# Kernel optimization log

Hardware: AMD Instinct MI355X
Metric: run time of the kernel (lower is better)

## Reference

```python
import jax, jax.numpy as jnp
import numpy as np

ALPHA_1 = 1.0
ALPHA_2 = 1.0

def setup_inputs() -> dict:
    key = jax.random.key(0)
    k1, k2, k3, k4 = jax.random.split(key, 4)
    n, d = 4096, 1024
    # xavier_normal-ish scale for (d,d): std = sqrt(2/(d+d)) = 1/sqrt(d)
    s = 1.0 / np.sqrt(d)
    Y = jax.random.normal(k1, (n, d), dtype=jnp.float32)
    W = jax.random.normal(k2, (d, d), dtype=jnp.float32) * s
    Wf = jax.random.normal(k3, (d, d), dtype=jnp.float32) * s
    B = jax.random.normal(k4, (1, d), dtype=jnp.float32) * s
    return {"Y": Y, "W": W, "Wf": Wf, "B": B}

def reference(Y, W, Wf, B):
    # Attention: scores = Y @ (W^T W) @ Y^T = (Y W^T)(Y W^T)^T
    YWt = Y @ W.T                      # (n, d)
    A = jax.nn.softmax(YWt @ YWt.T, axis=-1)  # (n, n)
    Z = (1.0 - ALPHA_1) * Y + ALPHA_1 * (A @ Y)  # (n, d); alpha_1=1 -> A@Y
    # FFN: Wf_eff = -0.5*alpha_2*(Wf + Wf^T) + (1-alpha_2)*I; alpha_2=1
    d = Wf.shape[0]
    Wf_eff = -0.5 * ALPHA_2 * (Wf + Wf.T) + (1.0 - ALPHA_2) * jnp.eye(d, dtype=Wf.dtype)
    out = Z @ Wf_eff + B               # (n, d)
    out = jax.nn.relu(out)             # relu=True
    return out
```

## Files before the change

### kernel.cpp

```cpp
#include <hip/hip_runtime.h>
#include <cstdint>
#include <cmath>


typedef __attribute__((ext_vector_type(8))) short short8;
typedef __attribute__((ext_vector_type(4))) short short4v;
typedef __attribute__((ext_vector_type(4))) float f32x4;

__device__ __forceinline__ short f2bf(float x) {
    unsigned u = __builtin_bit_cast(unsigned, x);
    u += 0x7fffu + ((u >> 16) & 1u);
    return (short)(u >> 16);
}
__device__ __forceinline__ float bf2f(short s) {
    unsigned u = ((unsigned)(unsigned short)s) << 16;
    return __builtin_bit_cast(float, u);
}

typedef const __attribute__((address_space(1))) void* gas1_t;
typedef __attribute__((address_space(3))) void* las3_t;
__device__ __forceinline__ void cp16(const void* g, void* l) {
    __builtin_amdgcn_global_load_lds((gas1_t)(uintptr_t)g, (las3_t)(uintptr_t)l, 16, 0, 0);
}

template<bool SPLIT, int OUTMODE, bool SYMM>
__global__ __launch_bounds__(256)
void mfma_gemm(const short* __restrict__ Ah, const short* __restrict__ Al,
               const short* __restrict__ Bh, const short* __restrict__ Bl,
               const float* __restrict__ bias, void* Co_, void* Cl_,
               int M, int N, int K)
{
    constexpr int BK = SPLIT ? 32 : 64;
    constexpr int NT = SPLIT ? 4 : 2;
    constexpr int TS = 128 * BK;
    __shared__ short lds[2][NT][TS];

    const int tid  = threadIdx.x;
    const int lane = tid & 63;
    const int wave = tid >> 6;
    const int wr   = wave >> 1, wc = wave & 1;

    int bm, bn, bi = 0, bj = 0;
    if (SYMM) {
        const int NB = N >> 7;
        int lin = blockIdx.x;
        const int nwg = gridDim.x;
        if ((nwg & 7) == 0) lin = (lin & 7) * (nwg >> 3) + (lin >> 3);
        const float ff = (float)(2 * NB + 1);
        int i = (int)((ff - sqrtf(ff * ff - 8.0f * (float)lin)) * 0.5f);
        while ((i + 1) * (2 * NB - i) / 2 <= lin) ++i;
        while (i * (2 * NB - i + 1) / 2 > lin) --i;
        bi = i;
        bj = i + (lin - i * (2 * NB - i + 1) / 2);
        bm = bi << 7; bn = bj << 7;
    } else {
        const int gx  = gridDim.x;
        const int nwg = gx * gridDim.y;
        int lin = blockIdx.y * gx + blockIdx.x;
        if ((nwg & 7) == 0) { const int cpx = nwg >> 3; lin = (lin & 7) * cpx + (lin >> 3); }
        bm = (lin / gx) << 7;
        bn = (lin % gx) << 7;
    }

    f32x4 acc[4][4];
#pragma unroll
    for (int i = 0; i < 4; ++i)
#pragma unroll
        for (int j = 0; j < 4; ++j)
#pragma unroll
            for (int q = 0; q < 4; ++q) acc[i][j][q] = 0.f;

    const short *pA0, *pA1, *pA2, *pA3, *pB0, *pB1, *pB2, *pB3;
    if constexpr (SPLIT) {
        const int srow = tid >> 2;
        const int csw  = (tid & 3) ^ ((tid >> 3) & 3);
        const size_t oA = (size_t)(bm + srow) * K + csw * 8;
        const size_t oB = (size_t)(bn + srow) * K + csw * 8;
        pA0 = Ah + oA; pA1 = Ah + oA + (size_t)64 * K;
        pA2 = Al + oA; pA3 = Al + oA + (size_t)64 * K;
        pB0 = Bh + oB; pB1 = Bh + oB + (size_t)64 * K;
        pB2 = Bl + oB; pB3 = Bl + oB + (size_t)64 * K;
    } else {
        const int srow = tid >> 3;
        const int lch  = (tid & 7) ^ (srow & 7);
        const size_t oA = (size_t)(bm + srow) * K + lch * 8;
        const size_t oB = (size_t)(bn + srow) * K + lch * 8;
        pA0 = Ah + oA; pA1 = pA0 + (size_t)32 * K;
        pA2 = pA0 + (size_t)64 * K; pA3 = pA0 + (size_t)96 * K;
        pB0 = Bh + oB; pB1 = pB0 + (size_t)32 * K;
        pB2 = pB0 + (size_t)64 * K; pB3 = pB0 + (size_t)96 * K;
    }

    auto stage = [&](int buf, int t) {
        short* db = &lds[buf][0][0] + tid * 8;
        const int ko = t * BK;
        if constexpr (SPLIT) {
            cp16(pA0 + ko, db);                cp16(pA1 + ko, db + 2048);
            cp16(pA2 + ko, db + 4096);         cp16(pA3 + ko, db + 4096 + 2048);
            cp16(pB0 + ko, db + 8192);         cp16(pB1 + ko, db + 8192 + 2048);
            cp16(pB2 + ko, db + 12288);        cp16(pB3 + ko, db + 12288 + 2048);
        } else {
            cp16(pA0 + ko, db);         cp16(pA1 + ko, db + 2048);
            cp16(pA2 + ko, db + 4096);  cp16(pA3 + ko, db + 6144);
            cp16(pB0 + ko, db + 8192);  cp16(pB1 + ko, db + 8192 + 2048);
            cp16(pB2 + ko, db + 8192 + 4096);  cp16(pB3 + ko, db + 8192 + 6144);
        }
    };

    int aoff, boff;
    if constexpr (SPLIT) {
        const int fsw = ((lane >> 4) ^ ((lane >> 1) & 3)) * 8;
        aoff = (wr * 64 + (lane & 15)) * 32 + fsw;
        boff = (wc * 64 + (lane & 15)) * 32 + fsw;
    } else {
        aoff = (wr * 64 + (lane & 15)) * 64;
        boff = (wc * 64 + (lane & 15)) * 64;
    }

    const int nt = K / BK;
    int cur = 0;

    stage(0, 0);
    asm volatile("s_waitcnt vmcnt(0)" ::: "memory");
    __syncthreads();

    for (int t = 0; t < nt; ++t) {
        if (t + 1 < nt) stage(cur ^ 1, t + 1);
        const short* base = &lds[cur][0][0];
        if constexpr (SPLIT) {
            short8 fah[4], fal[4], fbh[4], fbl[4];
#pragma unroll
            for (int i = 0; i < 4; ++i) {
                fah[i] = *(const short8*)(base + aoff + i * 512);
                fal[i] = *(const short8*)(base + 4096 + aoff + i * 512);
            }
#pragma unroll
            for (int j = 0; j < 4; ++j) {
                fbh[j] = *(const short8*)(base + 8192 + boff + j * 512);
                fbl[j] = *(const short8*)(base + 12288 + boff + j * 512);
            }
#pragma unroll
            for (int i = 0; i < 4; ++i)
#pragma unroll
                for (int j = 0; j < 4; ++j) {
                    acc[i][j] = __builtin_amdgcn_mfma_f32_16x16x32_bf16(fah[i], fbh[j], acc[i][j], 0, 0, 0);
                    acc[i][j] = __builtin_amdgcn_mfma_f32_16x16x32_bf16(fah[i], fbl[j], acc[i][j], 0, 0, 0);
                    acc[i][j] = __builtin_amdgcn_mfma_f32_16x16x32_bf16(fal[i], fbh[j], acc[i][j], 0, 0, 0);
                }
        } else {
#pragma unroll
            for (int ks = 0; ks < 2; ++ks) {
                const int sw = ((ks * 4 + (lane >> 4)) ^ (lane & 7)) * 8;
                short8 fa[4], fb[4];
#pragma unroll
                for (int i = 0; i < 4; ++i)
                    fa[i] = *(const short8*)(base + aoff + sw + i * 1024);
#pragma unroll
                for (int j = 0; j < 4; ++j)
                    fb[j] = *(const short8*)(base + 8192 + boff + sw + j * 1024);
#pragma unroll
                for (int i = 0; i < 4; ++i)
#pragma unroll
                    for (int j = 0; j < 4; ++j)
                        acc[i][j] = __builtin_amdgcn_mfma_f32_16x16x32_bf16(fa[i], fb[j], acc[i][j], 0, 0, 0);
            }
        }
        asm volatile("s_waitcnt vmcnt(0)" ::: "memory");
        __syncthreads();
        cur ^= 1;
    }

    const int crow0 = bm + wr * 64 + ((lane >> 4) << 2);
    const int ccol0 = bn + wc * 64 + (lane & 15);
    if constexpr (OUTMODE == 2) {
        float* C = (float*)Co_;
#pragma unroll
        for (int j = 0; j < 4; ++j) {
            const int c = ccol0 + j * 16;
            const float bv = bias[c];
#pragma unroll
            for (int i = 0; i < 4; ++i)
#pragma unroll
                for (int q = 0; q < 4; ++q) {
                    const int r = crow0 + i * 16 + q;
                    C[(size_t)r * N + c] = fmaxf(acc[i][j][q] + bv, 0.f);
                }
        }
    } else if constexpr (OUTMODE == 1) {
        short* Ch = (short*)Co_;
#pragma unroll
        for (int j = 0; j < 4; ++j) {
            const int c = ccol0 + j * 16;
#pragma unroll
            for (int i = 0; i < 4; ++i)
#pragma unroll
                for (int q = 0; q < 4; ++q) {
                    const int r = crow0 + i * 16 + q;
                    Ch[(size_t)r * N + c] = f2bf(acc[i][j][q]);
                }
        }
    } else {
        short* Ch = (short*)Co_;
        short* Cl = (short*)Cl_;
        const bool mirror = SYMM && (bi != bj);
#pragma unroll
        for (int j = 0; j < 4; ++j) {
            const int c = ccol0 + j * 16;
#pragma unroll
            for (int i = 0; i < 4; ++i)
#pragma unroll
                for (int q = 0; q < 4; ++q) {
                    const int r = crow0 + i * 16 + q;
                    const float v = acc[i][j][q];
                    const short hh = f2bf(v);
                    const short ll = f2bf(v - bf2f(hh));
                    Ch[(size_t)r * N + c] = hh;
                    Cl[(size_t)r * N + c] = ll;
                    if (mirror) {
                        Ch[(size_t)c * N + r] = hh;
                        Cl[(size_t)c * N + r] = ll;
                    }
                }
        }
    }
}

__global__ __launch_bounds__(256)
void softmax_hi(short* __restrict__ Shi, const short* __restrict__ Slo)
{
    const int row = blockIdx.x;
    short8* ph = (short8*)(Shi + (size_t)row * 4096);
    const short8* pl = (const short8*)(Slo + (size_t)row * 4096);
    const int t = threadIdx.x;

    short8 h0 = ph[t], h1 = ph[t + 256];
    short8 l0 = pl[t], l1 = pl[t + 256];
    float x[16];
#pragma unroll
    for (int j = 0; j < 8; ++j) {
        x[j]     = bf2f(h0[j]) + bf2f(l0[j]);
        x[8 + j] = bf2f(h1[j]) + bf2f(l1[j]);
    }
    float mx = x[0];
#pragma unroll
    for (int j = 1; j < 16; ++j) mx = fmaxf(mx, x[j]);
#pragma unroll
    for (int off = 32; off > 0; off >>= 1) mx = fmaxf(mx, __shfl_xor(mx, off));

    __shared__ float rm[4], rs[4];
    const int wv = t >> 6, ln = t & 63;
    if (ln == 0) rm[wv] = mx;
    __syncthreads();
    mx = fmaxf(fmaxf(rm[0], rm[1]), fmaxf(rm[2], rm[3]));

    float s = 0.f;
#pragma unroll
    for (int j = 0; j < 16; ++j) { x[j] = __expf(x[j] - mx); s += x[j]; }
#pragma unroll
    for (int off = 32; off > 0; off >>= 1) s += __shfl_xor(s, off);
    if (ln == 0) rs[wv] = s;
    __syncthreads();
    s = rs[0] + rs[1] + rs[2] + rs[3];

    const float inv = 1.f / s;
    short8 o0, o1;
#pragma unroll
    for (int j = 0; j < 8; ++j) {
        o0[j] = f2bf(x[j] * inv);
        o1[j] = f2bf(x[8 + j] * inv);
    }
    ph[t] = o0; ph[t + 256] = o1;
}

__global__ __launch_bounds__(256)
void split_y(const float* __restrict__ Y, short* __restrict__ Yhi,
             short* __restrict__ Ylo, short* __restrict__ Yt)
{
    __shared__ float tb[64][65];
    const int rb = blockIdx.y * 64, cb = blockIdx.x * 64;
    const int t = threadIdx.x;
    const int r = t >> 4, c4 = (t & 15) * 4;
#pragma unroll
    for (int it = 0; it < 4; ++it) {
        const int row = rb + r + it * 16;
        const float4 v = *(const float4*)&Y[(size_t)row * 1024 + cb + c4];
        const float f[4] = {v.x, v.y, v.z, v.w};
        short4v h, l;
#pragma unroll
        for (int k = 0; k < 4; ++k) {
            const short hh = f2bf(f[k]);
            h[k] = hh;
            l[k] = f2bf(f[k] - bf2f(hh));
        }
        *(short4v*)&Yhi[(size_t)row * 1024 + cb + c4] = h;
        *(short4v*)&Ylo[(size_t)row * 1024 + cb + c4] = l;
        tb[r + it * 16][c4 + 0] = v.x; tb[r + it * 16][c4 + 1] = v.y;
        tb[r + it * 16][c4 + 2] = v.z; tb[r + it * 16][c4 + 3] = v.w;
    }
    __syncthreads();
    const int orow = t >> 2, oc0 = (t & 3) * 16;
    short8 h8[2];
#pragma unroll
    for (int g = 0; g < 2; ++g)
#pragma unroll
        for (int j = 0; j < 8; ++j)
            h8[g][j] = f2bf(tb[oc0 + g * 8 + j][orow]);
    const size_t ob = (size_t)(cb + orow) * 4096 + rb + oc0;
    *(short8*)&Yt[ob] = h8[0];
    *(short8*)&Yt[ob + 8] = h8[1];
}

__global__ __launch_bounds__(256)
void split_w(const float* __restrict__ Wm, short* __restrict__ Wh, short* __restrict__ Wl)
{
    const size_t idx = ((size_t)blockIdx.x * 256 + threadIdx.x) * 4;
    const float4 v = *(const float4*)&Wm[idx];
    const float f[4] = {v.x, v.y, v.z, v.w};
    short4v h, l;
#pragma unroll
    for (int k = 0; k < 4; ++k) {
        const short hh = f2bf(f[k]);
        h[k] = hh;
        l[k] = f2bf(f[k] - bf2f(hh));
    }
    *(short4v*)&Wh[idx] = h;
    *(short4v*)&Wl[idx] = l;
}

__global__ __launch_bounds__(256)
void symm_hi(const float* __restrict__ Wf, short* __restrict__ Fh)
{
    const int i  = blockIdx.x;
    const int j0 = threadIdx.x * 4;
    const float4 rv = *(const float4*)&Wf[(size_t)i * 1024 + j0];
    const float c0 = Wf[(size_t)(j0 + 0) * 1024 + i];
    const float c1 = Wf[(size_t)(j0 + 1) * 1024 + i];
    const float c2 = Wf[(size_t)(j0 + 2) * 1024 + i];
    const float c3 = Wf[(size_t)(j0 + 3) * 1024 + i];
    short4v h;
    h[0] = f2bf(-0.5f * (rv.x + c0));
    h[1] = f2bf(-0.5f * (rv.y + c1));
    h[2] = f2bf(-0.5f * (rv.z + c2));
    h[3] = f2bf(-0.5f * (rv.w + c3));
    *(short4v*)&Fh[(size_t)i * 1024 + j0] = h;
}

extern "C" void kernel_launch(void* const* d_in, const int* in_sizes, int n_in,
                              void* d_out, int out_size, void* d_ws, size_t ws_size,
                              hipStream_t stream)
{
    const float* Y  = (const float*)d_in[0];
    const float* W  = (const float*)d_in[1];
    const float* Wf = (const float*)d_in[2];
    const float* Bb = (const float*)d_in[3];
    float* out = (float*)d_out;

    const int n = 4096, d = 1024;

    char* w = (char*)d_ws;
    short* Ythi = (short*)w; w += (size_t)d * n * 2;
    short* Wfeh = (short*)w; w += (size_t)d * d * 2;
    short* YWth = (short*)w; w += (size_t)n * d * 2;
    short* YWtl = (short*)w; w += (size_t)n * d * 2;
    short* Shi  = (short*)w; w += (size_t)n * n * 2;
    short* Slo  = (short*)w; w += (size_t)n * n * 2;
    short* Yhi = Shi;
    short* Ylo = Yhi + (size_t)n * d;
    short* Whi = Ylo + (size_t)n * d;
    short* Wlo = Whi + (size_t)d * d;
    short* Zhi = YWth;

    split_y<<<dim3(16, 64), 256, 0, stream>>>(Y, Yhi, Ylo, Ythi);
    split_w<<<dim3(1024), 256, 0, stream>>>(W, Whi, Wlo);
    symm_hi<<<dim3(1024), 256, 0, stream>>>(Wf, Wfeh);

    mfma_gemm<true, 0, false><<<dim3(8, 32), 256, 0, stream>>>(
        Yhi, Ylo, Whi, Wlo, nullptr, YWth, YWtl, n, d, d);

    mfma_gemm<true, 0, true><<<dim3(528), 256, 0, stream>>>(
        YWth, YWtl, YWth, YWtl, nullptr, Shi, Slo, n, n, d);

    softmax_hi<<<dim3(n), 256, 0, stream>>>(Shi, Slo);

    mfma_gemm<false, 1, false><<<dim3(8, 32), 256, 0, stream>>>(
        Shi, nullptr, Ythi, nullptr, nullptr, Zhi, nullptr, n, d, n);

    mfma_gemm<false, 2, false><<<dim3(8, 32), 256, 0, stream>>>(
        Zhi, nullptr, Wfeh, nullptr, Bb, out, nullptr, n, d, d);
}
```

Before: 306.4 us.

## Use 8-wave 512-thread GEMM blocks with 64x32 per-wave tiles

```diff
diff --git a/kernel.cpp b/kernel.cpp
--- a/kernel.cpp
+++ b/kernel.cpp
@@ -24,21 +24,20 @@
 }
 
 template<bool SPLIT, int OUTMODE, bool SYMM>
-__global__ __launch_bounds__(256)
+__global__ __launch_bounds__(512, 4)
 void mfma_gemm(const short* __restrict__ Ah, const short* __restrict__ Al,
                const short* __restrict__ Bh, const short* __restrict__ Bl,
                const float* __restrict__ bias, void* Co_, void* Cl_,
                int M, int N, int K)
 {
     constexpr int BK = SPLIT ? 32 : 64;
-    constexpr int NT = SPLIT ? 4 : 2;
-    constexpr int TS = 128 * BK;
-    __shared__ short lds[2][NT][TS];
+    __shared__ short lds[2][16384];
 
     const int tid  = threadIdx.x;
     const int lane = tid & 63;
     const int wave = tid >> 6;
-    const int wr   = wave >> 1, wc = wave & 1;
+    const int wr   = wave >> 2;
+    const int wc   = wave & 3;
 
     int bm, bn, bi = 0, bj = 0;
     if (SYMM) {
@@ -62,59 +61,48 @@
         bn = (lin % gx) << 7;
     }
 
-    f32x4 acc[4][4];
-#pragma unroll
-    for (int i = 0; i < 4; ++i)
-#pragma unroll
-        for (int j = 0; j < 4; ++j)
-#pragma unroll
-            for (int q = 0; q < 4; ++q) acc[i][j][q] = 0.f;
-
-    const short *pA0, *pA1, *pA2, *pA3, *pB0, *pB1, *pB2, *pB3;
+    f32x4 acc[4][2];
+#pragma unroll
+    for (int m = 0; m < 4; ++m)
+#pragma unroll
+        for (int n = 0; n < 2; ++n)
+#pragma unroll
+            for (int q = 0; q < 4; ++q) acc[m][n][q] = 0.f;
+
+    const short *pA0, *pA1, *pB0, *pB1;
     if constexpr (SPLIT) {
-        const int srow = tid >> 2;
-        const int csw  = (tid & 3) ^ ((tid >> 3) & 3);
-        const size_t oA = (size_t)(bm + srow) * K + csw * 8;
-        const size_t oB = (size_t)(bn + srow) * K + csw * 8;
-        pA0 = Ah + oA; pA1 = Ah + oA + (size_t)64 * K;
-        pA2 = Al + oA; pA3 = Al + oA + (size_t)64 * K;
-        pB0 = Bh + oB; pB1 = Bh + oB + (size_t)64 * K;
-        pB2 = Bl + oB; pB3 = Bl + oB + (size_t)64 * K;
+        const int row = tid >> 2;
+        const int csw = (tid & 3) ^ ((tid >> 3) & 3);
+        const size_t oA = (size_t)(bm + row) * K + csw * 8;
+        const size_t oB = (size_t)(bn + row) * K + csw * 8;
+        pA0 = Ah + oA; pA1 = Al + oA;
+        pB0 = Bh + oB; pB1 = Bl + oB;
     } else {
-        const int srow = tid >> 3;
-        const int lch  = (tid & 7) ^ (srow & 7);
-        const size_t oA = (size_t)(bm + srow) * K + lch * 8;
-        const size_t oB = (size_t)(bn + srow) * K + lch * 8;
-        pA0 = Ah + oA; pA1 = pA0 + (size_t)32 * K;
-        pA2 = pA0 + (size_t)64 * K; pA3 = pA0 + (size_t)96 * K;
-        pB0 = Bh + oB; pB1 = pB0 + (size_t)32 * K;
-        pB2 = pB0 + (size_t)64 * K; pB3 = pB0 + (size_t)96 * K;
+        const int row = tid >> 3;
+        const int lch = (tid & 7) ^ ((tid >> 3) & 7);
+        const size_t oA = (size_t)(bm + row) * K + lch * 8;
+        const size_t oB = (size_t)(bn + row) * K + lch * 8;
+        pA0 = Ah + oA; pA1 = pA0 + (size_t)64 * K;
+        pB0 = Bh + oB; pB1 = pB0 + (size_t)64 * K;
     }
 
     auto stage = [&](int buf, int t) {
-        short* db = &lds[buf][0][0] + tid * 8;
+        short* db = &lds[buf][0] + tid * 8;
         const int ko = t * BK;
-        if constexpr (SPLIT) {
-            cp16(pA0 + ko, db);                cp16(pA1 + ko, db + 2048);
-            cp16(pA2 + ko, db + 4096);         cp16(pA3 + ko, db + 4096 + 2048);
-            cp16(pB0 + ko, db + 8192);         cp16(pB1 + ko, db + 8192 + 2048);
-            cp16(pB2 + ko, db + 12288);        cp16(pB3 + ko, db + 12288 + 2048);
-        } else {
-            cp16(pA0 + ko, db);         cp16(pA1 + ko, db + 2048);
-            cp16(pA2 + ko, db + 4096);  cp16(pA3 + ko, db + 6144);
-            cp16(pB0 + ko, db + 8192);  cp16(pB1 + ko, db + 8192 + 2048);
-            cp16(pB2 + ko, db + 8192 + 4096);  cp16(pB3 + ko, db + 8192 + 6144);
-        }
+        cp16(pA0 + ko, db);
+        cp16(pA1 + ko, db + 4096);
+        cp16(pB0 + ko, db + 8192);
+        cp16(pB1 + ko, db + 12288);
     };
 
     int aoff, boff;
     if constexpr (SPLIT) {
-        const int fsw = ((lane >> 4) ^ ((lane >> 1) & 3)) * 8;
-        aoff = (wr * 64 + (lane & 15)) * 32 + fsw;
-        boff = (wc * 64 + (lane & 15)) * 32 + fsw;
+        const int swz = ((lane >> 4) ^ ((lane >> 1) & 3)) * 8;
+        aoff = (wr * 64 + (lane & 15)) * 32 + swz;
+        boff = (wc * 32 + (lane & 15)) * 32 + swz;
     } else {
         aoff = (wr * 64 + (lane & 15)) * 64;
-        boff = (wc * 64 + (lane & 15)) * 64;
+        boff = (wc * 32 + (lane & 15)) * 64;
     }
 
     const int nt = K / BK;
@@ -126,43 +114,41 @@
 
     for (int t = 0; t < nt; ++t) {
         if (t + 1 < nt) stage(cur ^ 1, t + 1);
-        const short* base = &lds[cur][0][0];
+        const short* base = &lds[cur][0];
         if constexpr (SPLIT) {
-            short8 fah[4], fal[4], fbh[4], fbl[4];
-#pragma unroll
-            for (int i = 0; i < 4; ++i) {
-                fah[i] = *(const short8*)(base + aoff + i * 512);
-                fal[i] = *(const short8*)(base + 4096 + aoff + i * 512);
+            short8 fah[4], fal[4];
+#pragma unroll
+            for (int m = 0; m < 4; ++m) {
+                fah[m] = *(const short8*)(base + aoff + m * 512);
+                fal[m] = *(const short8*)(base + 4096 + aoff + m * 512);
             }
 #pragma unroll
-            for (int j = 0; j < 4; ++j) {
-                fbh[j] = *(const short8*)(base + 8192 + boff + j * 512);
-                fbl[j] = *(const short8*)(base + 12288 + boff + j * 512);
+            for (int n = 0; n < 2; ++n) {
+                const short8 fbh = *(const short8*)(base + 8192 + boff + n * 512);
+                const short8 fbl = *(const short8*)(base + 12288 + boff + n * 512);
+#pragma unroll
+                for (int m = 0; m < 4; ++m) {
+                    acc[m][n] = __builtin_amdgcn_mfma_f32_16x16x32_bf16(fah[m], fbh, acc[m][n], 0, 0, 0);
+                    acc[m][n] = __builtin_amdgcn_mfma_f32_16x16x32_bf16(fah[m], fbl, acc[m][n], 0, 0, 0);
+                    acc[m][n] = __builtin_amdgcn_mfma_f32_16x16x32_bf16(fal[m], fbh, acc[m][n], 0, 0, 0);
+                }
             }
-#pragma unroll
-            for (int i = 0; i < 4; ++i)
-#pragma unroll
-                for (int j = 0; j < 4; ++j) {
-                    acc[i][j] = __builtin_amdgcn_mfma_f32_16x16x32_bf16(fah[i], fbh[j], acc[i][j], 0, 0, 0);
-                    acc[i][j] = __builtin_amdgcn_mfma_f32_16x16x32_bf16(fah[i], fbl[j], acc[i][j], 0, 0, 0);
-                    acc[i][j] = __builtin_amdgcn_mfma_f32_16x16x32_bf16(fal[i], fbh[j], acc[i][j], 0, 0, 0);
-                }
         } else {
 #pragma unroll
             for (int ks = 0; ks < 2; ++ks) {
                 const int sw = ((ks * 4 + (lane >> 4)) ^ (lane & 7)) * 8;
-                short8 fa[4], fb[4];
-#pragma unroll
-                for (int i = 0; i < 4; ++i)
-                    fa[i] = *(const short8*)(base + aoff + sw + i * 1024);
-#pragma unroll
-                for (int j = 0; j < 4; ++j)
-                    fb[j] = *(const short8*)(base + 8192 + boff + sw + j * 1024);
-#pragma unroll
-                for (int i = 0; i < 4; ++i)
-#pragma unroll
-                    for (int j = 0; j < 4; ++j)
-                        acc[i][j] = __builtin_amdgcn_mfma_f32_16x16x32_bf16(fa[i], fb[j], acc[i][j], 0, 0, 0);
+                short8 fa[4], fb[2];
+#pragma unroll
+                for (int m = 0; m < 4; ++m)
+                    fa[m] = *(const short8*)(base + aoff + sw + m * 1024);
+#pragma unroll
+                for (int n = 0; n < 2; ++n)
+                    fb[n] = *(const short8*)(base + 8192 + boff + sw + n * 1024);
+#pragma unroll
+                for (int m = 0; m < 4; ++m)
+#pragma unroll
+                    for (int n = 0; n < 2; ++n)
+                        acc[m][n] = __builtin_amdgcn_mfma_f32_16x16x32_bf16(fa[m], fb[n], acc[m][n], 0, 0, 0);
             }
         }
         asm volatile("s_waitcnt vmcnt(0)" ::: "memory");
@@ -171,32 +157,32 @@
     }
 
     const int crow0 = bm + wr * 64 + ((lane >> 4) << 2);
-    const int ccol0 = bn + wc * 64 + (lane & 15);
+    const int ccol0 = bn + wc * 32 + (lane & 15);
     if constexpr (OUTMODE == 2) {
         float* C = (float*)Co_;
 #pragma unroll
-        for (int j = 0; j < 4; ++j) {
-            const int c = ccol0 + j * 16;
+        for (int n = 0; n < 2; ++n) {
+            const int c = ccol0 + n * 16;
             const float bv = bias[c];
 #pragma unroll
-            for (int i = 0; i < 4; ++i)
+            for (int m = 0; m < 4; ++m)
 #pragma unroll
                 for (int q = 0; q < 4; ++q) {
-                    const int r = crow0 + i * 16 + q;
-                    C[(size_t)r * N + c] = fmaxf(acc[i][j][q] + bv, 0.f);
+                    const int r = crow0 + m * 16 + q;
+                    C[(size_t)r * N + c] = fmaxf(acc[m][n][q] + bv, 0.f);
                 }
         }
     } else if constexpr (OUTMODE == 1) {
         short* Ch = (short*)Co_;
 #pragma unroll
-        for (int j = 0; j < 4; ++j) {
-            const int c = ccol0 + j * 16;
-#pragma unroll
-            for (int i = 0; i < 4; ++i)
+        for (int n = 0; n < 2; ++n) {
+            const int c = ccol0 + n * 16;
+#pragma unroll
+            for (int m = 0; m < 4; ++m)
 #pragma unroll
                 for (int q = 0; q < 4; ++q) {
-                    const int r = crow0 + i * 16 + q;
-                    Ch[(size_t)r * N + c] = f2bf(acc[i][j][q]);
+                    const int r = crow0 + m * 16 + q;
+                    Ch[(size_t)r * N + c] = f2bf(acc[m][n][q]);
                 }
         }
     } else {
@@ -204,14 +190,14 @@
         short* Cl = (short*)Cl_;
         const bool mirror = SYMM && (bi != bj);
 #pragma unroll
-        for (int j = 0; j < 4; ++j) {
-            const int c = ccol0 + j * 16;
-#pragma unroll
-            for (int i = 0; i < 4; ++i)
+        for (int n = 0; n < 2; ++n) {
+            const int c = ccol0 + n * 16;
+#pragma unroll
+            for (int m = 0; m < 4; ++m)
 #pragma unroll
                 for (int q = 0; q < 4; ++q) {
-                    const int r = crow0 + i * 16 + q;
-                    const float v = acc[i][j][q];
+                    const int r = crow0 + m * 16 + q;
+                    const float v = acc[m][n][q];
                     const short hh = f2bf(v);
                     const short ll = f2bf(v - bf2f(hh));
                     Ch[(size_t)r * N + c] = hh;
@@ -374,17 +360,17 @@
     split_w<<<dim3(1024), 256, 0, stream>>>(W, Whi, Wlo);
     symm_hi<<<dim3(1024), 256, 0, stream>>>(Wf, Wfeh);
 
-    mfma_gemm<true, 0, false><<<dim3(8, 32), 256, 0, stream>>>(
+    mfma_gemm<true, 0, false><<<dim3(8, 32), 512, 0, stream>>>(
         Yhi, Ylo, Whi, Wlo, nullptr, YWth, YWtl, n, d, d);
 
-    mfma_gemm<true, 0, true><<<dim3(528), 256, 0, stream>>>(
+    mfma_gemm<true, 0, true><<<dim3(528), 512, 0, stream>>>(
         YWth, YWtl, YWth, YWtl, nullptr, Shi, Slo, n, n, d);
 
     softmax_hi<<<dim3(n), 256, 0, stream>>>(Shi, Slo);
 
-    mfma_gemm<false, 1, false><<<dim3(8, 32), 256, 0, stream>>>(
+    mfma_gemm<false, 1, false><<<dim3(8, 32), 512, 0, stream>>>(
         Shi, nullptr, Ythi, nullptr, nullptr, Zhi, nullptr, n, d, n);
 
-    mfma_gemm<false, 2, false><<<dim3(8, 32), 256, 0, stream>>>(
+    mfma_gemm<false, 2, false><<<dim3(8, 32), 512, 0, stream>>>(
         Zhi, nullptr, Wfeh, nullptr, Bb, out, nullptr, n, d, d);
 }
```

New measurement: 306.2 us. About the same (-0.1%).
